# Optimization experiments

Hardware: AMD Instinct MI355X
Metric: run time of the kernel (lower is better)

The kernel has to match this reference:

```python
import jax, jax.numpy as jnp
import numpy as np

DEPTH = 18                 # tree levels (complete binary tree, heap layout)
N = 2**DEPTH - 1           # 262143 nodes
X_SIZE = 128
H_SIZE = 128
VOCAB = 32000


def setup_inputs() -> dict:
    key = jax.random.key(0)
    ks = jax.random.split(key, 8)
    g = lambda k, shp, sc: jax.random.normal(k, shp, dtype=jnp.float32) * sc
    return {
        "x": jax.random.randint(ks[0], (N,), 0, VOCAB, dtype=jnp.int32),
        "mask": jax.random.randint(ks[1], (N,), 0, 2, dtype=jnp.int32),
        "E": g(ks[2], (VOCAB, X_SIZE), 0.02),
        "W_iou": g(ks[3], (X_SIZE, 3 * H_SIZE), X_SIZE ** -0.5),
        "b_iou_x": jnp.zeros((3 * H_SIZE,), jnp.float32),
        "W_f": g(ks[4], (X_SIZE, H_SIZE), X_SIZE ** -0.5),
        "b_f_x": jnp.zeros((H_SIZE,), jnp.float32),
        "U_iou": g(ks[5], (H_SIZE, 3 * H_SIZE), H_SIZE ** -0.5),
        "b_iou_h": jnp.zeros((3 * H_SIZE,), jnp.float32),
        "U_f": g(ks[6], (H_SIZE, H_SIZE), H_SIZE ** -0.5),
        "b_f_h": jnp.zeros((H_SIZE,), jnp.float32),
    }


def reference(x, mask, E, W_iou, b_iou_x, W_f, b_f_x, U_iou, b_iou_h, U_f, b_f_h):
    # input_module: embedding lookup of masked token ids
    m = mask.astype(jnp.float32)[:, None]                      # [N,1]
    embeds = E[x * mask]                                       # [N,X]
    iou_in = (embeds @ W_iou + b_iou_x) * m                    # [N,3H] gated per node
    f_in = (embeds @ W_f + b_f_x) * m                          # [N,H]

    Hd = U_f.shape[0]
    h = jnp.zeros((N, Hd), jnp.float32)
    c = jnp.zeros((N, Hd), jnp.float32)

    # topological propagation: leaves -> root (prop_nodes_topo)
    for lvl in range(DEPTH - 1, -1, -1):
        s0, e0 = 2 ** lvl - 1, 2 ** (lvl + 1) - 1              # node range at this level
        iou = iou_in[s0:e0] + b_iou_h                          # apply_node bias
        if lvl == DEPTH - 1:
            c_agg = jnp.zeros((e0 - s0, Hd), jnp.float32)      # leaves: no children
        else:
            # children of node i are 2i+1 (left) and 2i+2 (right): strided gather
            hl, hr = h[2 * s0 + 1:2 * e0:2], h[2 * s0 + 2:2 * e0 + 1:2]
            cl, cr = c[2 * s0 + 1:2 * e0:2], c[2 * s0 + 2:2 * e0 + 1:2]
            # per-child forget gates (child-sum aggregator, shared U_f)
            fl = jax.nn.sigmoid(f_in[s0:e0] + hl @ U_f + b_f_h)
            fr = jax.nn.sigmoid(f_in[s0:e0] + hr @ U_f + b_f_h)
            c_agg = fl * cl + fr * cr
            iou = iou + (hl + hr) @ U_iou
        i, o, u = jnp.split(iou, 3, axis=-1)
        c_new = jax.nn.sigmoid(i) * jnp.tanh(u) + c_agg
        h_new = jax.nn.sigmoid(o) * jnp.tanh(c_new)
        h = h.at[s0:e0].set(h_new)                             # scatter back to parents
        c = c.at[s0:e0].set(c_new)
    return h                                                   # output_module = identity
```

## Files before the change

kernel.cpp:

```cpp
#include <hip/hip_runtime.h>
#include <math.h>

typedef unsigned short u16;
typedef unsigned int u32;
typedef float f32x4 __attribute__((ext_vector_type(4)));
typedef short bfrag __attribute__((ext_vector_type(8)));

#define HS 128
#define DPLANE 4096000
#define DHB    33554304

__device__ __forceinline__ float sigf(float x) { return 1.0f / (1.0f + __expf(-x)); }
__device__ __forceinline__ float tanhfast(float x) {
    float e = __expf(2.0f * x);
    return 1.0f - 2.0f / (e + 1.0f);
}
__device__ __forceinline__ u16 f2bf(float f) {
    u32 u = __float_as_uint(f);
    return (u16)((u + 0x7FFFu + ((u >> 16) & 1u)) >> 16);
}
__device__ __forceinline__ float bf2f(u16 h) { return __uint_as_float(((u32)h) << 16); }

template<int N> __device__ __forceinline__ void waitv() {
    asm volatile("s_waitcnt vmcnt(%0)" :: "i"(N) : "memory");
}

__device__ __forceinline__ float bval_int(int k, int col,
    const float* W_iou, const float* W_f, const float* U_iou, const float* U_f)
{
    if (col < 384) {
        if (k < 128) return W_iou[k * 384 + col];
        if (k < 256) return U_iou[(k - 128) * 384 + col];
        return U_iou[(k - 256) * 384 + col];
    } else if (col < 512) {
        int cc = col - 384;
        if (k < 128) return W_f[k * 128 + cc];
        if (k < 256) return U_f[(k - 128) * 128 + cc];
        return 0.0f;
    } else {
        int cc = col - 512;
        if (k < 128) return W_f[k * 128 + cc];
        if (k < 256) return 0.0f;
        return U_f[(k - 256) * 128 + cc];
    }
}

#define TOT_INT (12 * 40 * 2 * 512)
#define TOT_LEAF (4 * 24 * 2 * 512)
#define ZBF_OFF (TOT_INT + TOT_LEAF)
#define EPL_OFF (ZBF_OFF + 128)
#define TOT_E 4096000
#define ZBP_OFF (EPL_OFF + TOT_E)
#define PREP_ALL (ZBP_OFF + 128)

__global__ __launch_bounds__(256) void prep_kernel(
    const float* __restrict__ W_iou, const float* __restrict__ W_f,
    const float* __restrict__ U_iou, const float* __restrict__ U_f,
    const float* __restrict__ E,
    u16* __restrict__ Bint, u16* __restrict__ Bleaf,
    u16* __restrict__ EH, u16* __restrict__ EL,
    u16* __restrict__ zbp, float* __restrict__ zbf)
{
    int idx = blockIdx.x * 256 + threadIdx.x;
    if (idx < TOT_INT) {
        int j8 = idx & 7, l = (idx >> 3) & 63, half = (idx >> 9) & 1;
        int rest = idx >> 10;
        int cfabs = rest % 40, kc = rest / 40;
        int wq = cfabs / 5, g = cfabs % 5;
        int j = 16 * wq + (l & 15);
        int origcol = (g < 3) ? g * 128 + j : ((g == 3) ? 384 + j : 512 + j);
        int k = kc * 32 + (l >> 4) * 8 + j8;
        float v = bval_int(k, origcol, W_iou, W_f, U_iou, U_f);
        u16 hi = f2bf(v);
        Bint[idx] = half ? f2bf(v - bf2f(hi)) : hi;
    } else if (idx < TOT_INT + TOT_LEAF) {
        int i2 = idx - TOT_INT;
        int j8 = i2 & 7, l = (i2 >> 3) & 63, half = (i2 >> 9) & 1;
        int rest = i2 >> 10;
        int cfabs = rest % 24, kc = rest / 24;
        int wq = cfabs / 3, g = cfabs % 3;
        int origcol = g * 128 + 16 * wq + (l & 15);
        int k = kc * 32 + (l >> 4) * 8 + j8;
        float v = W_iou[k * 384 + origcol];
        u16 hi = f2bf(v);
        Bleaf[i2] = half ? f2bf(v - bf2f(hi)) : hi;
    } else if (idx < EPL_OFF) {
        zbf[idx - ZBF_OFF] = 0.0f;
    } else if (idx < ZBP_OFF) {
        int i3 = idx - EPL_OFF;
        float v = E[i3];
        u16 hi = f2bf(v);
        EH[i3] = hi;
        EL[i3] = f2bf(v - bf2f(hi));
    } else if (idx < PREP_ALL) {
        zbp[idx - ZBP_OFF] = 0;
    }
}

template<int NKC, int NCFA, int NCF, int MODE>
__device__ __forceinline__ void phase_gemm(
    f32x4 (&acc)[4][NCF],
    const int* __restrict__ x, const int* __restrict__ mask,
    const u16* __restrict__ EH, const u16* __restrict__ zbp,
    const u16* __restrict__ hbH,
    const u16* __restrict__ Bg,
    u16* ldsA, const u16* ldsP,
    int n0, int lastn, int t)
{
    constexpr int NB = 2 * NCF;
    const int l = t & 63, wq = t >> 6;
    const int lr = l & 15, lg = l >> 4;

    const u16 *ebp, *hb1p = nullptr, *hb2p = nullptr;
    {
        const int prow = t & 63, pk8 = ((t >> 6) & 3) * 8, pp = t >> 8;
        int ns = n0 + prow; if (ns >= lastn) ns = n0;
        const u16* Ep = pp ? (EH + DPLANE) : EH;
        ebp = (mask[ns] ? Ep + (size_t)x[ns] * HS : zbp) + pk8;
        if (MODE == 1) {
            const u16* hbp = pp ? (hbH + DHB) : hbH;
            hb1p = hbp + (size_t)(2 * ns + 1) * HS + pk8;
            hb2p = hbp + (size_t)(2 * ns + 2) * HS + pk8;
        }
    }
    auto stageA = [&](int kc, int buf) {
        const u16* src;
        if (MODE == 1) {
            int seg = kc >> 2, ks = kc & 3;
            src = (seg == 0 ? ebp : (seg == 1 ? hb1p : hb2p)) + ks * 32;
        } else {
            src = ebp + (kc & 3) * 32;
        }
        __builtin_amdgcn_global_load_lds(
            (const __attribute__((address_space(1))) void*)src,
            (__attribute__((address_space(3))) void*)(ldsA + buf * 4096 + t * 8), 16, 0, 0);
    };
    const u16* bbase = Bg + (size_t)(wq * NCF) * 1024 + (size_t)l * 8;
    auto loadB = [&](int kc, bfrag (&bh)[NCF], bfrag (&bl)[NCF]) {
        const u16* bp = bbase + (size_t)kc * ((size_t)NCFA * 1024);
#pragma unroll
        for (int cf = 0; cf < NCF; ++cf) {
            bh[cf] = *(const bfrag*)(bp + (size_t)cf * 1024);
            bl[cf] = *(const bfrag*)(bp + (size_t)cf * 1024 + 512);
        }
    };
    auto compute = [&](int kk, bfrag (&bh)[NCF], bfrag (&bl)[NCF]) {
        bfrag ah[4], al[4];
        if (MODE == 2 && kk >= 4) {
            const int seg = (kk - 4) >> 2;
            const int kk8 = ((kk - 4) & 3) * 4 + lg;
#pragma unroll
            for (int rf = 0; rf < 4; ++rf) {
                int arow = 16 * rf + lr;
                ah[rf] = *(const bfrag*)(ldsP + ((size_t)kk8 * 128 + seg * 64 + arow) * 8);
                al[rf] = *(const bfrag*)(ldsP + ((size_t)(16 + kk8) * 128 + seg * 64 + arow) * 8);
            }
        } else {
            const u16* ab = ldsA + (kk % 3) * 4096;
#pragma unroll
            for (int rf = 0; rf < 4; ++rf) {
                int arow = 16 * rf + lr;
                ah[rf] = *(const bfrag*)(ab + ((size_t)lg * 64 + arow) * 8);
                al[rf] = *(const bfrag*)(ab + ((size_t)(4 + lg) * 64 + arow) * 8);
            }
        }
#pragma unroll
        for (int cf = 0; cf < NCF; ++cf) {
#pragma unroll
            for (int rf = 0; rf < 4; ++rf)
                acc[rf][cf] = __builtin_amdgcn_mfma_f32_16x16x32_bf16(ah[rf], bh[cf], acc[rf][cf], 0, 0, 0);
#pragma unroll
            for (int rf = 0; rf < 4; ++rf)
                acc[rf][cf] = __builtin_amdgcn_mfma_f32_16x16x32_bf16(al[rf], bh[cf], acc[rf][cf], 0, 0, 0);
#pragma unroll
            for (int rf = 0; rf < 4; ++rf)
                acc[rf][cf] = __builtin_amdgcn_mfma_f32_16x16x32_bf16(ah[rf], bl[cf], acc[rf][cf], 0, 0, 0);
        }
    };

    bfrag bhA[NCF], blA[NCF], bhB[NCF], blB[NCF];
    stageA(0, 0);
    loadB(0, bhA, blA);
    stageA(1, 1);

#pragma unroll 1
    for (int kc = 0; kc < NKC; kc += 2) {
        loadB(kc + 1, bhB, blB);
        if constexpr (MODE == 2) { if (kc <= 2) waitv<NB + 1>(); else waitv<NB>(); }
        else waitv<NB + 1>();
        __builtin_amdgcn_s_barrier();
        asm volatile("" ::: "memory");
        if constexpr (MODE == 2) { if (kc + 2 < 4) stageA(kc + 2, (kc + 2) % 3); }
        else                     { if (kc + 2 <= NKC - 1) stageA(kc + 2, (kc + 2) % 3); }
        compute(kc, bhA, blA);

        { int kn = kc + 2; if (kn > NKC - 1) kn = NKC - 1; loadB(kn, bhA, blA); }
        if constexpr (MODE == 2) { if (kc == 0) waitv<NB + 1>(); else waitv<NB>(); }
        else { if (kc == NKC - 2) waitv<NB>(); else waitv<NB + 1>(); }
        __builtin_amdgcn_s_barrier();
        asm volatile("" ::: "memory");
        if constexpr (MODE == 2) { if (kc + 3 < 4) stageA(kc + 3, (kc + 3) % 3); }
        else                     { if (kc + 3 <= NKC - 1) stageA(kc + 3, (kc + 3) % 3); }
        compute(kc + 1, bhB, blB);
    }
}

template<int NCF, bool LEAF>
__device__ __forceinline__ void child_epilogue(
    f32x4 (&acc)[4][NCF],
    const int* __restrict__ mask,
    const float* __restrict__ b_iou_x, const float* __restrict__ b_f_x,
    const float* __restrict__ b_iou_h, const float* __restrict__ b_f_h,
    float* __restrict__ h, const float* __restrict__ c,
    u16* ldsP, float* ldsC,
    int n0, int lastn, int oBase, int t)
{
    const int l = t & 63, wq = t >> 6, lr = l & 15, lg = l >> 4;
    const int j = 16 * wq + lr;
    float bix = b_iou_x[j], box = b_iou_x[HS + j], bux = b_iou_x[2 * HS + j];
    float bih = b_iou_h[j], boh = b_iou_h[HS + j], buh = b_iou_h[2 * HS + j];
    float bfx = 0.0f, bfh = 0.0f;
    if constexpr (!LEAF) { bfx = b_f_x[j]; bfh = b_f_h[j]; }
#pragma unroll
    for (int rf = 0; rf < 4; ++rf) {
#pragma unroll
        for (int r = 0; r < 4; ++r) {
            int ctr = 16 * rf + 4 * lg + r;
            int n = n0 + ctr;
            if (n >= lastn) continue;
            float m = (float)mask[n];
            float iv = acc[rf][0][r] + m * bix + bih;
            float ov = acc[rf][1][r] + m * box + boh;
            float uv = acc[rf][2][r] + m * bux + buh;
            float cn;
            if constexpr (!LEAF) {
                float fl = acc[rf][3][r] + m * bfx + bfh;
                float fr = acc[rf][4][r] + m * bfx + bfh;
                float cl = c[(size_t)(2 * n + 1) * HS + j];
                float cr = c[(size_t)(2 * n + 2) * HS + j];
                cn = sigf(iv) * tanhfast(uv) + sigf(fl) * cl + sigf(fr) * cr;
            } else {
                cn = sigf(iv) * tanhfast(uv);
            }
            float hn = sigf(ov) * tanhfast(cn);
            h[(size_t)n * HS + j] = hn;
            int o = oBase + ctr;
            int half = o & 1, slot = o >> 1;
            u16 hh = f2bf(hn);
            ldsP[((size_t)(j >> 3) * 128 + half * 64 + slot) * 8 + (j & 7)] = hh;
            ldsP[((size_t)(16 + (j >> 3)) * 128 + half * 64 + slot) * 8 + (j & 7)] = f2bf(hn - bf2f(hh));
            ldsC[o * 129 + j] = cn;
        }
    }
}

__device__ __forceinline__ void parent_epilogue(
    f32x4 (&acc)[4][5],
    const int* __restrict__ mask,
    const float* __restrict__ b_iou_x, const float* __restrict__ b_f_x,
    const float* __restrict__ b_iou_h, const float* __restrict__ b_f_h,
    float* __restrict__ h, float* __restrict__ c, u16* __restrict__ hbH,
    const float* ldsC,
    int n0, int lastn, int t)
{
    u16* hbL = hbH + DHB;
    const int l = t & 63, wq = t >> 6, lr = l & 15, lg = l >> 4;
    const int j = 16 * wq + lr;
    float bix = b_iou_x[j], box = b_iou_x[HS + j], bux = b_iou_x[2 * HS + j];
    float bih = b_iou_h[j], boh = b_iou_h[HS + j], buh = b_iou_h[2 * HS + j];
    float bfx = b_f_x[j], bfh = b_f_h[j];
#pragma unroll
    for (int rf = 0; rf < 4; ++rf) {
#pragma unroll
        for (int r = 0; r < 4; ++r) {
            int ctr = 16 * rf + 4 * lg + r;
            int n = n0 + ctr;
            if (n >= lastn) continue;
            float m = (float)mask[n];
            float iv = acc[rf][0][r] + m * bix + bih;
            float ov = acc[rf][1][r] + m * box + boh;
            float uv = acc[rf][2][r] + m * bux + buh;
            float fl = acc[rf][3][r] + m * bfx + bfh;
            float fr = acc[rf][4][r] + m * bfx + bfh;
            float cl = ldsC[(2 * ctr) * 129 + j];
            float cr = ldsC[(2 * ctr + 1) * 129 + j];
            float cn = sigf(iv) * tanhfast(uv) + sigf(fl) * cl + sigf(fr) * cr;
            float hn = sigf(ov) * tanhfast(cn);
            c[(size_t)n * HS + j] = cn;
            h[(size_t)n * HS + j] = hn;
            u16 hh = f2bf(hn);
            hbH[(size_t)n * HS + j] = hh;
            hbL[(size_t)n * HS + j] = f2bf(hn - bf2f(hh));
        }
    }
}

template<bool LEAFCH>
__global__ __launch_bounds__(512, 2) void fused_pair(
    const int* __restrict__ x, const int* __restrict__ mask,
    const u16* __restrict__ EH, const u16* __restrict__ zbp,
    const u16* __restrict__ Bint, const u16* __restrict__ Bleaf,
    const float* __restrict__ b_iou_x, const float* __restrict__ b_f_x,
    const float* __restrict__ b_iou_h, const float* __restrict__ b_f_h,
    float* __restrict__ h, float* __restrict__ c, u16* __restrict__ hbH,
    int s0p, int Mp)
{
    __shared__ __align__(16) u16 ldsA[3 * 4096];
    __shared__ __align__(16) u16 ldsP[2 * 16 * 128 * 8];
    __shared__ __align__(16) float ldsC[128 * 129];
    const int t = threadIdx.x;
    const int p0 = s0p + blockIdx.x * 64;
    const int lastp = s0p + Mp;
    const int lastc = 2 * lastp + 1;

    constexpr int CNCF = LEAFCH ? 3 : 5;
    const f32x4 zzz = {0.0f, 0.0f, 0.0f, 0.0f};

    {
        f32x4 acc[4][CNCF];
#pragma unroll
        for (int rf = 0; rf < 4; ++rf)
#pragma unroll
            for (int cf = 0; cf < CNCF; ++cf) acc[rf][cf] = zzz;
        phase_gemm<LEAFCH ? 4 : 12, LEAFCH ? 24 : 40, CNCF, LEAFCH ? 0 : 1>(
            acc, x, mask, EH, zbp, hbH, LEAFCH ? Bleaf : Bint, ldsA, ldsP, 2 * p0 + 1, lastc, t);
        child_epilogue<CNCF, LEAFCH>(acc, mask, b_iou_x, b_f_x, b_iou_h, b_f_h,
                                     h, c, ldsP, ldsC, 2 * p0 + 1, lastc, 0, t);
    }
    __syncthreads();
    {
        f32x4 acc[4][CNCF];
#pragma unroll
        for (int rf = 0; rf < 4; ++rf)
#pragma unroll
            for (int cf = 0; cf < CNCF; ++cf) acc[rf][cf] = zzz;
        phase_gemm<LEAFCH ? 4 : 12, LEAFCH ? 24 : 40, CNCF, LEAFCH ? 0 : 1>(
            acc, x, mask, EH, zbp, hbH, LEAFCH ? Bleaf : Bint, ldsA, ldsP, 2 * p0 + 65, lastc, t);
        child_epilogue<CNCF, LEAFCH>(acc, mask, b_iou_x, b_f_x, b_iou_h, b_f_h,
                                     h, c, ldsP, ldsC, 2 * p0 + 65, lastc, 64, t);
    }
    __syncthreads();
    {
        f32x4 acc[4][5];
#pragma unroll
        for (int rf = 0; rf < 4; ++rf)
#pragma unroll
            for (int cf = 0; cf < 5; ++cf) acc[rf][cf] = zzz;
        phase_gemm<12, 40, 5, 2>(acc, x, mask, EH, zbp, hbH, Bint, ldsA, ldsP, p0, lastp, t);
        parent_epilogue(acc, mask, b_iou_x, b_f_x, b_iou_h, b_f_h,
                        h, c, hbH, ldsC, p0, lastp, t);
    }
}

#define TAIL_BLOCKS 40

__device__ __forceinline__ void grid_barrier(u32* ctr, u32 target, int t) {
    __syncthreads();
    if (t == 0) {
        __threadfence();
        __hip_atomic_fetch_add(ctr, 1u, __ATOMIC_RELEASE, __HIP_MEMORY_SCOPE_AGENT);
        while (__hip_atomic_load(ctr, __ATOMIC_ACQUIRE, __HIP_MEMORY_SCOPE_AGENT) < target)
            __builtin_amdgcn_s_sleep(4);
        __threadfence();
    }
    __syncthreads();
}

__global__ __launch_bounds__(512, 2) void tail_kernel(
    const int* __restrict__ x, const int* __restrict__ mask,
    const u16* __restrict__ EH, const u16* __restrict__ zbp,
    const u16* __restrict__ Bint,
    const float* __restrict__ b_iou_x, const float* __restrict__ b_f_x,
    const float* __restrict__ b_iou_h, const float* __restrict__ b_f_h,
    float* __restrict__ h, float* __restrict__ c, u16* __restrict__ hbH,
    u32* __restrict__ bar)
{
    __shared__ __align__(16) u16 ldsB[120 * 512];
    __shared__ __align__(16) u16 ldsA[2 * 8192];
    const int t = threadIdx.x;
    const int wq = blockIdx.x & 7;
    const int rg = blockIdx.x >> 3;
    const int l = t & 63, w = t >> 6;
    const int lr = l & 15, lg = l >> 4;
    u16* hbL = hbH + DHB;

    for (int rr = 0; rr < 15; ++rr) {
        int s = rr * 8 + w;
        int kcq = s / 10, rem = s % 10, cf = rem >> 1, half = rem & 1;
        const u16* src = Bint + ((size_t)((kcq * 40 + wq * 5 + cf) * 2 + half)) * 512 + l * 8;
        *(bfrag*)(ldsB + (size_t)s * 512 + l * 8) = *(const bfrag*)src;
    }
    __syncthreads();

    const int j = 16 * wq + lr;
    const float bix = b_iou_x[j], box = b_iou_x[HS + j], bux = b_iou_x[2 * HS + j];
    const float bih = b_iou_h[j], boh = b_iou_h[HS + j], buh = b_iou_h[2 * HS + j];
    const float bfx = b_f_x[j], bfh = b_f_h[j];

    const int row = t & 127, kslot = (t >> 7) & 3;
    const f32x4 zzz = {0.0f, 0.0f, 0.0f, 0.0f};

#pragma unroll 1
    for (int lvl = 11; lvl >= 0; --lvl) {
        const int s0 = (1 << lvl) - 1, M = 1 << lvl;
        const int lastn = s0 + M;
        const int ntiles = (M + 127) >> 7;
#pragma unroll 1
        for (int tile = rg; tile < ntiles; tile += 5) {
            const int n0 = s0 + tile * 128;
            int ns = n0 + row; if (ns >= lastn) ns = n0;
            const int mk = mask[ns];
            const u16* pE = (mk ? EH + (size_t)x[ns] * HS : zbp) + kslot * 8;
            const int dE = mk ? DPLANE : 0;
            const u16* p1 = hbH + (size_t)(2 * ns + 1) * HS + kslot * 8;
            const u16* p2 = hbH + (size_t)(2 * ns + 2) * HS + kslot * 8;

            auto stageA = [&](int kc, int buf) {
                const u16 *sh; int dd;
                int ks = kc & 3;
                if (kc < 4)      { sh = pE + ks * 32; dd = dE; }
                else if (kc < 8) { sh = p1 + ks * 32; dd = DHB; }
                else             { sh = p2 + ks * 32; dd = DHB; }
                u16* d = ldsA + buf * 8192 + t * 8;
                __builtin_amdgcn_global_load_lds(
                    (const __attribute__((address_space(1))) void*)sh,
                    (__attribute__((address_space(3))) void*)d, 16, 0, 0);
                __builtin_amdgcn_global_load_lds(
                    (const __attribute__((address_space(1))) void*)(sh + dd),
                    (__attribute__((address_space(3))) void*)(d + 4096), 16, 0, 0);
            };

            f32x4 acc[5];
#pragma unroll
            for (int cf = 0; cf < 5; ++cf) acc[cf] = zzz;

            stageA(0, 0);
            stageA(1, 1);
#pragma unroll 1
            for (int kc = 0; kc < 12; ++kc) {
                if (kc < 11) waitv<2>(); else waitv<0>();
                __builtin_amdgcn_s_barrier();
                asm volatile("" ::: "memory");
                const u16* ab = ldsA + (kc & 1) * 8192;
                const int arow = 16 * w + lr;
                bfrag ah = *(const bfrag*)(ab + ((size_t)lg * 128 + arow) * 8);
                bfrag al = *(const bfrag*)(ab + ((size_t)(512 + lg * 128 + arow)) * 8);
                const u16* bb = ldsB + (size_t)kc * (10 * 512) + l * 8;
#pragma unroll
                for (int cf = 0; cf < 5; ++cf) {
                    bfrag bh = *(const bfrag*)(bb + (size_t)(2 * cf) * 512);
                    bfrag bl = *(const bfrag*)(bb + (size_t)(2 * cf + 1) * 512);
                    acc[cf] = __builtin_amdgcn_mfma_f32_16x16x32_bf16(ah, bh, acc[cf], 0, 0, 0);
                    acc[cf] = __builtin_amdgcn_mfma_f32_16x16x32_bf16(al, bh, acc[cf], 0, 0, 0);
                    acc[cf] = __builtin_amdgcn_mfma_f32_16x16x32_bf16(ah, bl, acc[cf], 0, 0, 0);
                }
                __builtin_amdgcn_s_barrier();
                asm volatile("" ::: "memory");
                if (kc + 2 < 12) stageA(kc + 2, kc & 1);
            }

#pragma unroll
            for (int r = 0; r < 4; ++r) {
                int n = n0 + 16 * w + 4 * lg + r;
                if (n >= lastn) continue;
                float m = (float)mask[n];
                float iv = acc[0][r] + m * bix + bih;
                float ov = acc[1][r] + m * box + boh;
                float uv = acc[2][r] + m * bux + buh;
                float fl = acc[3][r] + m * bfx + bfh;
                float fr = acc[4][r] + m * bfx + bfh;
                float cl = c[(size_t)(2 * n + 1) * HS + j];
                float cr = c[(size_t)(2 * n + 2) * HS + j];
                float cn = sigf(iv) * tanhfast(uv) + sigf(fl) * cl + sigf(fr) * cr;
                float hn = sigf(ov) * tanhfast(cn);
                c[(size_t)n * HS + j] = cn;
                h[(size_t)n * HS + j] = hn;
                u16 hh = f2bf(hn);
                hbH[(size_t)n * HS + j] = hh;
                hbL[(size_t)n * HS + j] = f2bf(hn - bf2f(hh));
            }
        }
        if (lvl > 0) grid_barrier(&bar[11 - lvl], TAIL_BLOCKS, t);
    }
}

extern "C" void kernel_launch(void* const* d_in, const int* in_sizes, int n_in,
                              void* d_out, int out_size, void* d_ws, size_t ws_size,
                              hipStream_t stream)
{
    const int*   x       = (const int*)d_in[0];
    const int*   mask    = (const int*)d_in[1];
    const float* E       = (const float*)d_in[2];
    const float* W_iou   = (const float*)d_in[3];
    const float* b_iou_x = (const float*)d_in[4];
    const float* W_f     = (const float*)d_in[5];
    const float* b_f_x   = (const float*)d_in[6];
    const float* U_iou   = (const float*)d_in[7];
    const float* b_iou_h = (const float*)d_in[8];
    const float* U_f     = (const float*)d_in[9];
    const float* b_f_h   = (const float*)d_in[10];

    float* h = (float*)d_out;
    char* ws = (char*)d_ws;

    u16*   Bint  = (u16*)(ws);
    u16*   Bleaf = (u16*)(ws + 983040);
    float* zbf   = (float*)(ws + 1179648);
    u32*   bar   = (u32*)(ws + 1179648);
    u16*   EH    = (u16*)(ws + 1180160);
    u16*   EL    = (u16*)(ws + 9372160);
    u16*   zbp   = (u16*)(ws + 17564160);
    float* c     = (float*)(ws + 17564416);
    u16*   hbH   = (u16*)(ws + 151781632);

    prep_kernel<<<PREP_ALL / 256, 256, 0, stream>>>(
        W_iou, W_f, U_iou, U_f, E, Bint, Bleaf, EH, EL, zbp, zbf);

    for (int lvl = 16; lvl >= 12; lvl -= 2) {
        int s0p = (1 << lvl) - 1, Mp = 1 << lvl;
        int blocks = (Mp + 63) / 64;
        if (lvl == 16)
            fused_pair<true><<<blocks, 512, 0, stream>>>(
                x, mask, EH, zbp, Bint, Bleaf,
                b_iou_x, b_f_x, b_iou_h, b_f_h, h, c, hbH, s0p, Mp);
        else
            fused_pair<false><<<blocks, 512, 0, stream>>>(
                x, mask, EH, zbp, Bint, Bleaf,
                b_iou_x, b_f_x, b_iou_h, b_f_h, h, c, hbH, s0p, Mp);
    }

    tail_kernel<<<TAIL_BLOCKS, 512, 0, stream>>>(
        x, mask, EH, zbp, Bint,
        b_iou_x, b_f_x, b_iou_h, b_f_h, h, c, hbH, bar);
}
```

Before: 619.9 us.

## Load A fragments directly into registers in tail kernel, dropping LDS staging

```diff
diff --git a/kernel.cpp b/kernel.cpp
--- a/kernel.cpp
+++ b/kernel.cpp
@@ -376,7 +376,6 @@
     u32* __restrict__ bar)
 {
     __shared__ __align__(16) u16 ldsB[120 * 512];
-    __shared__ __align__(16) u16 ldsA[2 * 8192];
     const int t = threadIdx.x;
     const int wq = blockIdx.x & 7;
     const int rg = blockIdx.x >> 3;
@@ -397,7 +396,6 @@
     const float bih = b_iou_h[j], boh = b_iou_h[HS + j], buh = b_iou_h[2 * HS + j];
     const float bfx = b_f_x[j], bfh = b_f_h[j];
 
-    const int row = t & 127, kslot = (t >> 7) & 3;
     const f32x4 zzz = {0.0f, 0.0f, 0.0f, 0.0f};
 
 #pragma unroll 1
@@ -408,55 +406,46 @@
 #pragma unroll 1
         for (int tile = rg; tile < ntiles; tile += 5) {
             const int n0 = s0 + tile * 128;
-            int ns = n0 + row; if (ns >= lastn) ns = n0;
-            const int mk = mask[ns];
-            const u16* pE = (mk ? EH + (size_t)x[ns] * HS : zbp) + kslot * 8;
+            int rowA = n0 + 16 * w + lr;
+            if (rowA >= lastn) rowA = n0;
+            const int mk = mask[rowA];
+            const u16* pE = (mk ? EH + (size_t)x[rowA] * HS : zbp) + lg * 8;
             const int dE = mk ? DPLANE : 0;
-            const u16* p1 = hbH + (size_t)(2 * ns + 1) * HS + kslot * 8;
-            const u16* p2 = hbH + (size_t)(2 * ns + 2) * HS + kslot * 8;
-
-            auto stageA = [&](int kc, int buf) {
-                const u16 *sh; int dd;
-                int ks = kc & 3;
-                if (kc < 4)      { sh = pE + ks * 32; dd = dE; }
-                else if (kc < 8) { sh = p1 + ks * 32; dd = DHB; }
-                else             { sh = p2 + ks * 32; dd = DHB; }
-                u16* d = ldsA + buf * 8192 + t * 8;
-                __builtin_amdgcn_global_load_lds(
-                    (const __attribute__((address_space(1))) void*)sh,
-                    (__attribute__((address_space(3))) void*)d, 16, 0, 0);
-                __builtin_amdgcn_global_load_lds(
-                    (const __attribute__((address_space(1))) void*)(sh + dd),
-                    (__attribute__((address_space(3))) void*)(d + 4096), 16, 0, 0);
-            };
+            const u16* p1 = hbH + (size_t)(2 * rowA + 1) * HS + lg * 8;
+            const u16* p2 = hbH + (size_t)(2 * rowA + 2) * HS + lg * 8;
+
+            bfrag ah[12], al[12];
+#pragma unroll
+            for (int kc = 0; kc < 4; ++kc) {
+                ah[kc] = *(const bfrag*)(pE + kc * 32);
+                al[kc] = *(const bfrag*)(pE + kc * 32 + dE);
+            }
+#pragma unroll
+            for (int kc = 0; kc < 4; ++kc) {
+                ah[4 + kc] = *(const bfrag*)(p1 + kc * 32);
+                al[4 + kc] = *(const bfrag*)(p1 + kc * 32 + DHB);
+            }
+#pragma unroll
+            for (int kc = 0; kc < 4; ++kc) {
+                ah[8 + kc] = *(const bfrag*)(p2 + kc * 32);
+                al[8 + kc] = *(const bfrag*)(p2 + kc * 32 + DHB);
+            }
 
             f32x4 acc[5];
 #pragma unroll
             for (int cf = 0; cf < 5; ++cf) acc[cf] = zzz;
 
-            stageA(0, 0);
-            stageA(1, 1);
-#pragma unroll 1
+#pragma unroll
             for (int kc = 0; kc < 12; ++kc) {
-                if (kc < 11) waitv<2>(); else waitv<0>();
-                __builtin_amdgcn_s_barrier();
-                asm volatile("" ::: "memory");
-                const u16* ab = ldsA + (kc & 1) * 8192;
-                const int arow = 16 * w + lr;
-                bfrag ah = *(const bfrag*)(ab + ((size_t)lg * 128 + arow) * 8);
-                bfrag al = *(const bfrag*)(ab + ((size_t)(512 + lg * 128 + arow)) * 8);
                 const u16* bb = ldsB + (size_t)kc * (10 * 512) + l * 8;
 #pragma unroll
                 for (int cf = 0; cf < 5; ++cf) {
                     bfrag bh = *(const bfrag*)(bb + (size_t)(2 * cf) * 512);
                     bfrag bl = *(const bfrag*)(bb + (size_t)(2 * cf + 1) * 512);
-                    acc[cf] = __builtin_amdgcn_mfma_f32_16x16x32_bf16(ah, bh, acc[cf], 0, 0, 0);
-                    acc[cf] = __builtin_amdgcn_mfma_f32_16x16x32_bf16(al, bh, acc[cf], 0, 0, 0);
-                    acc[cf] = __builtin_amdgcn_mfma_f32_16x16x32_bf16(ah, bl, acc[cf], 0, 0, 0);
+                    acc[cf] = __builtin_amdgcn_mfma_f32_16x16x32_bf16(ah[kc], bh, acc[cf], 0, 0, 0);
+                    acc[cf] = __builtin_amdgcn_mfma_f32_16x16x32_bf16(al[kc], bh, acc[cf], 0, 0, 0);
+                    acc[cf] = __builtin_amdgcn_mfma_f32_16x16x32_bf16(ah[kc], bl, acc[cf], 0, 0, 0);
                 }
-                __builtin_amdgcn_s_barrier();
-                asm volatile("" ::: "memory");
-                if (kc + 2 < 12) stageA(kc + 2, kc & 1);
             }
 
 #pragma unroll
```

After: 1.068 ms. +72.3%, slower.
